# Kernel optimization log

Measured on AMD Instinct MI355X. Metric: run time of the kernel, lower is better.

## Reference

```python
import jax, jax.numpy as jnp
import numpy as np

B, L, C, R = 64, 2048, 512, 64
EPS_NORM = 1e-12
EPS_LN = 1e-5


def setup_inputs() -> dict:
    key = jax.random.key(0)
    ks = jax.random.split(key, 12)
    s_in = 1.0 / np.sqrt(L)
    s_r = 1.0 / np.sqrt(R)
    return {
        "x": jax.random.normal(ks[0], (B, L, C), dtype=jnp.float32),
        "Wd": jax.random.uniform(ks[1], (R, L), jnp.float32, -s_in, s_in),
        "bd": jax.random.uniform(ks[2], (R,), jnp.float32, -s_in, s_in),
        "Wq": jax.random.uniform(ks[3], (R, R), jnp.float32, -s_r, s_r),
        "Wk": jax.random.uniform(ks[4], (R, R), jnp.float32, -s_r, s_r),
        "Wv": jax.random.uniform(ks[5], (R, R), jnp.float32, -s_r, s_r),
        "Wg": jax.random.uniform(ks[6], (R, R), jnp.float32, -s_r, s_r),
        "bg": jax.random.uniform(ks[7], (R,), jnp.float32, -s_r, s_r),
        "Wu": jax.random.uniform(ks[8], (L, R), jnp.float32, -s_r, s_r),
        "bu": jax.random.uniform(ks[9], (L,), jnp.float32, -s_r, s_r),
        "gamma": jnp.ones((C,), jnp.float32),
        "beta": jnp.zeros((C,), jnp.float32),
        "alpha": jnp.asarray(0.1, jnp.float32),
    }


def _l2norm(t):
    # F.normalize(p=2, dim=-1): x / max(||x||, eps)
    n = jnp.sqrt(jnp.sum(t * t, axis=-1, keepdims=True))
    return t / jnp.maximum(n, EPS_NORM)


def reference(x, Wd, bd, Wq, Wk, Wv, Wg, bg, Wu, bu, gamma, beta, alpha):
    h = jnp.swapaxes(x, 1, 2)                      # (B, C, L): C tokens, L features
    h_low = jnp.einsum('bcl,rl->bcr', h, Wd) + bd  # (B, C, R)
    Q = _l2norm(jnp.einsum('bcr,sr->bcs', h_low, Wq))
    K = _l2norm(jnp.einsum('bcr,sr->bcs', h_low, Wk))
    V = jnp.einsum('bcr,sr->bcs', h_low, Wv)
    global_feat = jnp.sum(K * V, axis=1, keepdims=True)  # (B, 1, R)
    h_attn = Q * global_feat
    gate = jax.nn.sigmoid(jnp.einsum('bcr,sr->bcs', h_low, Wg) + bg)
    h_attn = h_attn * gate
    h_mixed = jnp.einsum('bcr,lr->bcl', h_attn, Wu) + bu  # (B, C, L)
    out = h + alpha * h_mixed
    out = jnp.swapaxes(out, 1, 2)                  # (B, L, C)
    mu = jnp.mean(out, axis=-1, keepdims=True)
    var = jnp.mean((out - mu) ** 2, axis=-1, keepdims=True)
    return (out - mu) / jnp.sqrt(var + EPS_LN) * gamma + beta
```

## Files before the change

### kernel.cpp

```cpp
#include <hip/hip_runtime.h>
#include <hip/hip_bf16.h>
#include <math.h>

#define B_ 64
#define L_ 2048
#define C_ 512
#define R_ 64
#define TL 16

#define BM 128
#define BK 32
#define LDK 36

typedef __attribute__((ext_vector_type(8))) short bf16x8;
typedef __attribute__((ext_vector_type(4))) float f32x4;

static __device__ __forceinline__ unsigned pkbf(float a, float b) {
    __hip_bfloat162 t = __float22bfloat162_rn(make_float2(a, b));
    union { __hip_bfloat162 h; unsigned u; } cv;
    cv.h = t;
    return cv.u;
}

__global__ void k_cast_wd(const float* __restrict__ Wd,
                          __hip_bfloat16* __restrict__ Wt) {
    int i = blockIdx.x * 256 + threadIdx.x;
    Wt[i] = __float2bfloat16(Wd[i]);
}

__global__ __launch_bounds__(256) void k_hlow_mfma(
        const float* __restrict__ x,
        const __hip_bfloat16* __restrict__ Wt,
        float* __restrict__ hlT) {
    __shared__ float xs[BM][LDK];

    const int tid  = threadIdx.x;
    const int lane = tid & 63;
    const int wv   = tid >> 6;
    const int quad = lane >> 4;
    const int mrow = lane & 15;

    const int c0     = blockIdx.x * BM;
    const int l_base = blockIdx.y * (L_ / 2);
    const int b      = blockIdx.z;

    const int cs = tid & 127;
    const int lh = (tid >> 7) * 16;

    f32x4 acc[2][4];
#pragma unroll
    for (int mt = 0; mt < 2; ++mt)
#pragma unroll
        for (int nt = 0; nt < 4; ++nt)
#pragma unroll
            for (int e = 0; e < 4; ++e) acc[mt][nt][e] = 0.f;

    const float* xptr = x + ((size_t)b * L_ + l_base + lh) * C_ + c0 + cs;
    const __hip_bfloat16* wbase = Wt + l_base + quad * 8;

    for (int kc = 0; kc < L_ / 2; kc += BK) {
        float v[16];
#pragma unroll
        for (int i = 0; i < 16; ++i) v[i] = xptr[(size_t)(kc + i) * C_];

        bf16x8 bfr[4];
#pragma unroll
        for (int nt = 0; nt < 4; ++nt)
            bfr[nt] = *reinterpret_cast<const bf16x8*>(
                wbase + (size_t)(nt * 16 + mrow) * L_ + kc);

        __syncthreads();
#pragma unroll
        for (int i = 0; i < 16; i += 4)
            *reinterpret_cast<float4*>(&xs[cs][lh + i]) =
                make_float4(v[i], v[i + 1], v[i + 2], v[i + 3]);
        __syncthreads();

#pragma unroll
        for (int mt = 0; mt < 2; ++mt) {
            const float* ap = &xs[wv * 32 + mt * 16 + mrow][quad * 8];
            float4 lo = *reinterpret_cast<const float4*>(ap);
            float4 hi = *reinterpret_cast<const float4*>(ap + 4);
            union { bf16x8 v8; unsigned u[4]; } af;
            af.u[0] = pkbf(lo.x, lo.y);
            af.u[1] = pkbf(lo.z, lo.w);
            af.u[2] = pkbf(hi.x, hi.y);
            af.u[3] = pkbf(hi.z, hi.w);
#pragma unroll
            for (int nt = 0; nt < 4; ++nt)
                acc[mt][nt] = __builtin_amdgcn_mfma_f32_16x16x32_bf16(
                    af.v8, bfr[nt], acc[mt][nt], 0, 0, 0);
        }
    }

#pragma unroll
    for (int mt = 0; mt < 2; ++mt)
#pragma unroll
        for (int nt = 0; nt < 4; ++nt) {
            const int rg = nt * 16 + mrow;
            const int cg = c0 + wv * 32 + mt * 16 + quad * 4;
#pragma unroll
            for (int e = 0; e < 4; ++e)
                atomicAdd(&hlT[((size_t)b * R_ + rg) * C_ + cg + e],
                          acc[mt][nt][e]);
        }
}

__global__ __launch_bounds__(256) void k_qkvg(
        const float* __restrict__ hlT,
        const float* __restrict__ bd,
        const float* __restrict__ Wq,
        const float* __restrict__ Wk,
        const float* __restrict__ Wv,
        const float* __restrict__ Wg,
        const float* __restrict__ bg,
        float* __restrict__ PT,
        float* __restrict__ G) {
    const int lane = threadIdx.x & 63;
    const int wv   = threadIdx.x >> 6;
    const int c    = blockIdx.x * 64 + lane;
    const int b    = blockIdx.y;

    float h[R_];
#pragma unroll
    for (int r = 0; r < R_; ++r)
        h[r] = hlT[((size_t)b * R_ + r) * C_ + c] + bd[r];

    float sq = 0.f, sk = 0.f;
#pragma unroll 4
    for (int i = 0; i < 16; ++i) {
        const int s = wv * 16 + i;
        const float4* wq4 = reinterpret_cast<const float4*>(Wq + s * R_);
        const float4* wk4 = reinterpret_cast<const float4*>(Wk + s * R_);
        float q = 0.f, k = 0.f;
#pragma unroll
        for (int j = 0; j < R_ / 4; ++j) {
            float4 a = wq4[j], d = wk4[j];
            float h0 = h[4 * j], h1 = h[4 * j + 1], h2 = h[4 * j + 2], h3 = h[4 * j + 3];
            q += h0 * a.x + h1 * a.y + h2 * a.z + h3 * a.w;
            k += h0 * d.x + h1 * d.y + h2 * d.z + h3 * d.w;
        }
        sq += q * q;
        sk += k * k;
    }

    __shared__ float rq[4][64], rk[4][64];
    rq[wv][lane] = sq;
    rk[wv][lane] = sk;
    __syncthreads();
    sq = rq[0][lane] + rq[1][lane] + rq[2][lane] + rq[3][lane];
    sk = rk[0][lane] + rk[1][lane] + rk[2][lane] + rk[3][lane];
    const float inq = 1.f / fmaxf(sqrtf(sq), 1e-12f);
    const float ink = 1.f / fmaxf(sqrtf(sk), 1e-12f);

#pragma unroll 2
    for (int i = 0; i < 16; ++i) {
        const int s = wv * 16 + i;
        const float4* wq4 = reinterpret_cast<const float4*>(Wq + s * R_);
        const float4* wk4 = reinterpret_cast<const float4*>(Wk + s * R_);
        const float4* wv4 = reinterpret_cast<const float4*>(Wv + s * R_);
        const float4* wg4 = reinterpret_cast<const float4*>(Wg + s * R_);
        float q = 0.f, k = 0.f, v = 0.f, g = 0.f;
#pragma unroll
        for (int j = 0; j < R_ / 4; ++j) {
            float4 a = wq4[j], d = wk4[j], e = wv4[j], f = wg4[j];
            float h0 = h[4 * j], h1 = h[4 * j + 1], h2 = h[4 * j + 2], h3 = h[4 * j + 3];
            q += h0 * a.x + h1 * a.y + h2 * a.z + h3 * a.w;
            k += h0 * d.x + h1 * d.y + h2 * d.z + h3 * d.w;
            v += h0 * e.x + h1 * e.y + h2 * e.z + h3 * e.w;
            g += h0 * f.x + h1 * f.y + h2 * f.z + h3 * f.w;
        }
        const float gate = 1.f / (1.f + expf(-(g + bg[s])));
        PT[((size_t)b * R_ + s) * C_ + c] = q * inq * gate;

        float kv = (k * ink) * v;
#pragma unroll
        for (int off = 32; off > 0; off >>= 1) kv += __shfl_xor(kv, off, 64);
        if (lane == 0) atomicAdd(&G[b * R_ + s], kv);
    }
}

__global__ __launch_bounds__(512) void k_out(const float* __restrict__ x,
                                             const float* __restrict__ PT,
                                             const float* __restrict__ G,
                                             const float* __restrict__ Wu,
                                             const float* __restrict__ bu,
                                             const float* __restrict__ gamma,
                                             const float* __restrict__ beta,
                                             const float* __restrict__ alpha_p,
                                             float* __restrict__ out) {
    const int c  = threadIdx.x;
    const int b  = blockIdx.y;
    const int l0 = blockIdx.x * TL;
    const float alpha = alpha_p[0];

    float ha[R_];
#pragma unroll
    for (int r = 0; r < R_; ++r)
        ha[r] = PT[((size_t)b * R_ + r) * C_ + c] * G[b * R_ + r];

    float vals[TL];
#pragma unroll
    for (int lt = 0; lt < TL; ++lt) {
        const int l = l0 + lt;
        const float4* wu4 = reinterpret_cast<const float4*>(Wu + l * R_);
        float m = 0.f;
#pragma unroll
        for (int i = 0; i < R_ / 4; ++i) {
            float4 w = wu4[i];
            m += ha[4 * i] * w.x + ha[4 * i + 1] * w.y + ha[4 * i + 2] * w.z + ha[4 * i + 3] * w.w;
        }
        vals[lt] = x[((size_t)b * L_ + l) * C_ + c] + alpha * (m + bu[l]);
    }

    __shared__ float2 redLds[TL][8];
    __shared__ float2 mvLds[TL];
    const int lane = c & 63, wv = c >> 6;
#pragma unroll
    for (int lt = 0; lt < TL; ++lt) {
        float s = vals[lt], s2 = vals[lt] * vals[lt];
#pragma unroll
        for (int off = 32; off > 0; off >>= 1) {
            s  += __shfl_xor(s, off, 64);
            s2 += __shfl_xor(s2, off, 64);
        }
        if (lane == 0) redLds[lt][wv] = make_float2(s, s2);
    }
    __syncthreads();
    if (threadIdx.x < TL) {
        float s = 0.f, s2 = 0.f;
#pragma unroll
        for (int w = 0; w < 8; ++w) {
            s  += redLds[threadIdx.x][w].x;
            s2 += redLds[threadIdx.x][w].y;
        }
        const float mean = s * (1.f / C_);
        const float var  = s2 * (1.f / C_) - mean * mean;
        mvLds[threadIdx.x] = make_float2(mean, rsqrtf(var + 1e-5f));
    }
    __syncthreads();
    const float gm = gamma[c], bt = beta[c];
#pragma unroll
    for (int lt = 0; lt < TL; ++lt) {
        float2 mv = mvLds[lt];
        out[((size_t)b * L_ + (l0 + lt)) * C_ + c] = (vals[lt] - mv.x) * mv.y * gm + bt;
    }
}

extern "C" void kernel_launch(void* const* d_in, const int* in_sizes, int n_in,
                              void* d_out, int out_size, void* d_ws, size_t ws_size,
                              hipStream_t stream) {
    const float* x     = (const float*)d_in[0];
    const float* Wd    = (const float*)d_in[1];
    const float* bd    = (const float*)d_in[2];
    const float* Wq    = (const float*)d_in[3];
    const float* Wk    = (const float*)d_in[4];
    const float* Wv    = (const float*)d_in[5];
    const float* Wg    = (const float*)d_in[6];
    const float* bg    = (const float*)d_in[7];
    const float* Wu    = (const float*)d_in[8];
    const float* bu    = (const float*)d_in[9];
    const float* gamma = (const float*)d_in[10];
    const float* beta  = (const float*)d_in[11];
    const float* alpha = (const float*)d_in[12];
    float* out = (float*)d_out;

    char* ws = (char*)d_ws;
    __hip_bfloat16* Wt = (__hip_bfloat16*)ws;
    float* hlT = (float*)(ws + (512 << 10));
    float* PT  = (float*)(ws + (512 << 10) + (8 << 20));
    float* G   = (float*)(ws + (512 << 10) + (16 << 20));

    k_cast_wd<<<dim3((R_ * L_) / 256), 256, 0, stream>>>(Wd, Wt);
    hipMemsetAsync(hlT, 0, (size_t)B_ * R_ * C_ * sizeof(float), stream);
    hipMemsetAsync(G, 0, B_ * R_ * sizeof(float), stream);
    k_hlow_mfma<<<dim3(C_ / BM, 2, B_), 256, 0, stream>>>(x, Wt, hlT);
    k_qkvg<<<dim3(C_ / 64, B_), 256, 0, stream>>>(hlT, bd, Wq, Wk, Wv, Wg, bg, PT, G);
    k_out<<<dim3(L_ / TL, B_), 512, 0, stream>>>(x, PT, G, Wu, bu, gamma, beta, alpha, out);
}
```

Before: 804.7 us.

## Use bf16 MFMA for up-projection, transpose intermediates, split L across more blocks

The output kernel now computes the up-projection with bf16 MFMA instructions, using a pre-cast bf16 copy of Wu, instead of a scalar fp32 dot-product loop per thread. The h_low and P intermediates are stored row-major (C by R) so loads can be vectorised. The down-projection split-K grows from 2 to 8 slices to expose more parallelism, at the cost of more atomic adds. The qkvg kernel is restructured so each thread computes 8 output features with a single pass over the weights. The bf16 rounding of P·G and Wu adds some numerical error.

Result: faster. 741.2 us (-7.9%).

```diff
diff --git a/kernel.cpp b/kernel.cpp
--- a/kernel.cpp
+++ b/kernel.cpp
@@ -11,6 +11,8 @@
 #define BM 128
 #define BK 32
 #define LDK 36
+#define NSL 8
+#define LSL (L_ / NSL)
 
 typedef __attribute__((ext_vector_type(8))) short bf16x8;
 typedef __attribute__((ext_vector_type(4))) float f32x4;
@@ -22,16 +24,19 @@
     return cv.u;
 }
 
-__global__ void k_cast_wd(const float* __restrict__ Wd,
-                          __hip_bfloat16* __restrict__ Wt) {
+__global__ void k_cast(const float* __restrict__ Wd,
+                       const float* __restrict__ Wu,
+                       __hip_bfloat16* __restrict__ Wt,
+                       __hip_bfloat16* __restrict__ Wub) {
     int i = blockIdx.x * 256 + threadIdx.x;
-    Wt[i] = __float2bfloat16(Wd[i]);
+    if (i < R_ * L_) Wt[i] = __float2bfloat16(Wd[i]);
+    else             Wub[i - R_ * L_] = __float2bfloat16(Wu[i - R_ * L_]);
 }
 
 __global__ __launch_bounds__(256) void k_hlow_mfma(
         const float* __restrict__ x,
         const __hip_bfloat16* __restrict__ Wt,
-        float* __restrict__ hlT) {
+        float* __restrict__ hl) {
     __shared__ float xs[BM][LDK];
 
     const int tid  = threadIdx.x;
@@ -41,7 +46,7 @@
     const int mrow = lane & 15;
 
     const int c0     = blockIdx.x * BM;
-    const int l_base = blockIdx.y * (L_ / 2);
+    const int l_base = blockIdx.y * LSL;
     const int b      = blockIdx.z;
 
     const int cs = tid & 127;
@@ -58,7 +63,7 @@
     const float* xptr = x + ((size_t)b * L_ + l_base + lh) * C_ + c0 + cs;
     const __hip_bfloat16* wbase = Wt + l_base + quad * 8;
 
-    for (int kc = 0; kc < L_ / 2; kc += BK) {
+    for (int kc = 0; kc < LSL; kc += BK) {
         float v[16];
 #pragma unroll
         for (int i = 0; i < 16; ++i) v[i] = xptr[(size_t)(kc + i) * C_];
@@ -101,149 +106,198 @@
             const int cg = c0 + wv * 32 + mt * 16 + quad * 4;
 #pragma unroll
             for (int e = 0; e < 4; ++e)
-                atomicAdd(&hlT[((size_t)b * R_ + rg) * C_ + cg + e],
+                atomicAdd(&hl[((size_t)b * C_ + cg + e) * R_ + rg],
                           acc[mt][nt][e]);
         }
 }
 
 __global__ __launch_bounds__(256) void k_qkvg(
-        const float* __restrict__ hlT,
+        const float* __restrict__ hl,
         const float* __restrict__ bd,
         const float* __restrict__ Wq,
         const float* __restrict__ Wk,
         const float* __restrict__ Wv,
         const float* __restrict__ Wg,
         const float* __restrict__ bg,
-        float* __restrict__ PT,
+        float* __restrict__ P,
         float* __restrict__ G) {
-    const int lane = threadIdx.x & 63;
-    const int wv   = threadIdx.x >> 6;
-    const int c    = blockIdx.x * 64 + lane;
-    const int b    = blockIdx.y;
-
-    float h[R_];
-#pragma unroll
-    for (int r = 0; r < R_; ++r)
-        h[r] = hlT[((size_t)b * R_ + r) * C_ + c] + bd[r];
+    const int tid = threadIdx.x;
+    const int ci  = tid & 31;
+    const int sg  = tid >> 5;
+    const int wv  = tid >> 6;
+    const int c   = blockIdx.x * 32 + ci;
+    const int b   = blockIdx.y;
+    const int s0  = sg * 8;
+    const float* hrow = hl + ((size_t)b * C_ + c) * R_;
+
+    float q[8], k[8], v[8], g[8];
+#pragma unroll
+    for (int i = 0; i < 8; ++i) { q[i] = 0.f; k[i] = 0.f; v[i] = 0.f; g[i] = 0.f; }
+
+#pragma unroll 1
+    for (int jc = 0; jc < 4; ++jc) {
+        float hc[16];
+        const float4* h4 = reinterpret_cast<const float4*>(hrow + jc * 16);
+        const float4* b4 = reinterpret_cast<const float4*>(bd + jc * 16);
+#pragma unroll
+        for (int t = 0; t < 4; ++t) {
+            float4 hv = h4[t], bv = b4[t];
+            hc[4 * t + 0] = hv.x + bv.x;
+            hc[4 * t + 1] = hv.y + bv.y;
+            hc[4 * t + 2] = hv.z + bv.z;
+            hc[4 * t + 3] = hv.w + bv.w;
+        }
+#pragma unroll
+        for (int i = 0; i < 8; ++i) {
+            const float4* wq4 = reinterpret_cast<const float4*>(Wq + (size_t)(s0 + i) * R_ + jc * 16);
+            const float4* wk4 = reinterpret_cast<const float4*>(Wk + (size_t)(s0 + i) * R_ + jc * 16);
+            const float4* wv4 = reinterpret_cast<const float4*>(Wv + (size_t)(s0 + i) * R_ + jc * 16);
+            const float4* wg4 = reinterpret_cast<const float4*>(Wg + (size_t)(s0 + i) * R_ + jc * 16);
+#pragma unroll
+            for (int t = 0; t < 4; ++t) {
+                float4 a = wq4[t], d = wk4[t], e2 = wv4[t], f = wg4[t];
+                float h0 = hc[4 * t], h1 = hc[4 * t + 1], h2 = hc[4 * t + 2], h3 = hc[4 * t + 3];
+                q[i] += h0 * a.x  + h1 * a.y  + h2 * a.z  + h3 * a.w;
+                k[i] += h0 * d.x  + h1 * d.y  + h2 * d.z  + h3 * d.w;
+                v[i] += h0 * e2.x + h1 * e2.y + h2 * e2.z + h3 * e2.w;
+                g[i] += h0 * f.x  + h1 * f.y  + h2 * f.z  + h3 * f.w;
+            }
+        }
+    }
 
     float sq = 0.f, sk = 0.f;
-#pragma unroll 4
-    for (int i = 0; i < 16; ++i) {
-        const int s = wv * 16 + i;
-        const float4* wq4 = reinterpret_cast<const float4*>(Wq + s * R_);
-        const float4* wk4 = reinterpret_cast<const float4*>(Wk + s * R_);
-        float q = 0.f, k = 0.f;
-#pragma unroll
-        for (int j = 0; j < R_ / 4; ++j) {
-            float4 a = wq4[j], d = wk4[j];
-            float h0 = h[4 * j], h1 = h[4 * j + 1], h2 = h[4 * j + 2], h3 = h[4 * j + 3];
-            q += h0 * a.x + h1 * a.y + h2 * a.z + h3 * a.w;
-            k += h0 * d.x + h1 * d.y + h2 * d.z + h3 * d.w;
-        }
-        sq += q * q;
-        sk += k * k;
-    }
-
-    __shared__ float rq[4][64], rk[4][64];
-    rq[wv][lane] = sq;
-    rk[wv][lane] = sk;
+#pragma unroll
+    for (int i = 0; i < 8; ++i) { sq += q[i] * q[i]; sk += k[i] * k[i]; }
+    sq += __shfl_xor(sq, 32, 64);
+    sk += __shfl_xor(sk, 32, 64);
+    __shared__ float rqs[4][32], rks[4][32];
+    if ((tid & 32) == 0) { rqs[wv][ci] = sq; rks[wv][ci] = sk; }
     __syncthreads();
-    sq = rq[0][lane] + rq[1][lane] + rq[2][lane] + rq[3][lane];
-    sk = rk[0][lane] + rk[1][lane] + rk[2][lane] + rk[3][lane];
+    sq = rqs[0][ci] + rqs[1][ci] + rqs[2][ci] + rqs[3][ci];
+    sk = rks[0][ci] + rks[1][ci] + rks[2][ci] + rks[3][ci];
     const float inq = 1.f / fmaxf(sqrtf(sq), 1e-12f);
     const float ink = 1.f / fmaxf(sqrtf(sk), 1e-12f);
 
-#pragma unroll 2
-    for (int i = 0; i < 16; ++i) {
-        const int s = wv * 16 + i;
-        const float4* wq4 = reinterpret_cast<const float4*>(Wq + s * R_);
-        const float4* wk4 = reinterpret_cast<const float4*>(Wk + s * R_);
-        const float4* wv4 = reinterpret_cast<const float4*>(Wv + s * R_);
-        const float4* wg4 = reinterpret_cast<const float4*>(Wg + s * R_);
-        float q = 0.f, k = 0.f, v = 0.f, g = 0.f;
-#pragma unroll
-        for (int j = 0; j < R_ / 4; ++j) {
-            float4 a = wq4[j], d = wk4[j], e = wv4[j], f = wg4[j];
-            float h0 = h[4 * j], h1 = h[4 * j + 1], h2 = h[4 * j + 2], h3 = h[4 * j + 3];
-            q += h0 * a.x + h1 * a.y + h2 * a.z + h3 * a.w;
-            k += h0 * d.x + h1 * d.y + h2 * d.z + h3 * d.w;
-            v += h0 * e.x + h1 * e.y + h2 * e.z + h3 * e.w;
-            g += h0 * f.x + h1 * f.y + h2 * f.z + h3 * f.w;
-        }
-        const float gate = 1.f / (1.f + expf(-(g + bg[s])));
-        PT[((size_t)b * R_ + s) * C_ + c] = q * inq * gate;
-
-        float kv = (k * ink) * v;
-#pragma unroll
-        for (int off = 32; off > 0; off >>= 1) kv += __shfl_xor(kv, off, 64);
-        if (lane == 0) atomicAdd(&G[b * R_ + s], kv);
-    }
+    float pv[8], kv[8];
+#pragma unroll
+    for (int i = 0; i < 8; ++i) {
+        const float gate = 1.f / (1.f + expf(-(g[i] + bg[s0 + i])));
+        pv[i] = q[i] * inq * gate;
+        kv[i] = (k[i] * ink) * v[i];
+    }
+    float* prow = P + ((size_t)b * C_ + c) * R_ + s0;
+    *reinterpret_cast<float4*>(prow)     = make_float4(pv[0], pv[1], pv[2], pv[3]);
+    *reinterpret_cast<float4*>(prow + 4) = make_float4(pv[4], pv[5], pv[6], pv[7]);
+
+#pragma unroll
+    for (int off = 1; off < 32; off <<= 1)
+#pragma unroll
+        for (int i = 0; i < 8; ++i) kv[i] += __shfl_xor(kv[i], off, 64);
+    if (ci == 0)
+#pragma unroll
+        for (int i = 0; i < 8; ++i) atomicAdd(&G[b * R_ + s0 + i], kv[i]);
 }
 
 __global__ __launch_bounds__(512) void k_out(const float* __restrict__ x,
-                                             const float* __restrict__ PT,
+                                             const float* __restrict__ P,
                                              const float* __restrict__ G,
-                                             const float* __restrict__ Wu,
+                                             const __hip_bfloat16* __restrict__ Wub,
                                              const float* __restrict__ bu,
                                              const float* __restrict__ gamma,
                                              const float* __restrict__ beta,
                                              const float* __restrict__ alpha_p,
                                              float* __restrict__ out) {
-    const int c  = threadIdx.x;
-    const int b  = blockIdx.y;
-    const int l0 = blockIdx.x * TL;
+    const int tid  = threadIdx.x;
+    const int lane = tid & 63;
+    const int wv   = tid >> 6;
+    const int n16  = lane & 15;
+    const int quad = lane >> 4;
+    const int b    = blockIdx.y;
+    const int l0   = blockIdx.x * TL;
     const float alpha = alpha_p[0];
 
-    float ha[R_];
-#pragma unroll
-    for (int r = 0; r < R_; ++r)
-        ha[r] = PT[((size_t)b * R_ + r) * C_ + c] * G[b * R_ + r];
-
-    float vals[TL];
-#pragma unroll
-    for (int lt = 0; lt < TL; ++lt) {
-        const int l = l0 + lt;
-        const float4* wu4 = reinterpret_cast<const float4*>(Wu + l * R_);
-        float m = 0.f;
-#pragma unroll
-        for (int i = 0; i < R_ / 4; ++i) {
-            float4 w = wu4[i];
-            m += ha[4 * i] * w.x + ha[4 * i + 1] * w.y + ha[4 * i + 2] * w.z + ha[4 * i + 3] * w.w;
-        }
-        vals[lt] = x[((size_t)b * L_ + l) * C_ + c] + alpha * (m + bu[l]);
-    }
-
-    __shared__ float2 redLds[TL][8];
-    __shared__ float2 mvLds[TL];
-    const int lane = c & 63, wv = c >> 6;
-#pragma unroll
-    for (int lt = 0; lt < TL; ++lt) {
-        float s = vals[lt], s2 = vals[lt] * vals[lt];
-#pragma unroll
-        for (int off = 32; off > 0; off >>= 1) {
+    const __hip_bfloat16* wrow = Wub + (size_t)(l0 + n16) * R_ + quad * 8;
+    const bf16x8 af0 = *reinterpret_cast<const bf16x8*>(wrow);
+    const bf16x8 af1 = *reinterpret_cast<const bf16x8*>(wrow + 32);
+
+    const float* gp = G + b * R_ + quad * 8;
+    const float4 ga0 = *reinterpret_cast<const float4*>(gp);
+    const float4 ga1 = *reinterpret_cast<const float4*>(gp + 4);
+    const float4 gb0 = *reinterpret_cast<const float4*>(gp + 32);
+    const float4 gb1 = *reinterpret_cast<const float4*>(gp + 36);
+
+    f32x4 acc[4];
+#pragma unroll
+    for (int nt = 0; nt < 4; ++nt)
+#pragma unroll
+        for (int e = 0; e < 4; ++e) acc[nt][e] = 0.f;
+
+    const int cb = wv * 64;
+#pragma unroll
+    for (int nt = 0; nt < 4; ++nt) {
+        const float* prow = P + ((size_t)b * C_ + cb + nt * 16 + n16) * R_ + quad * 8;
+        float4 p0 = *reinterpret_cast<const float4*>(prow);
+        float4 p1 = *reinterpret_cast<const float4*>(prow + 4);
+        union { bf16x8 v8; unsigned u[4]; } bf;
+        bf.u[0] = pkbf(p0.x * ga0.x, p0.y * ga0.y);
+        bf.u[1] = pkbf(p0.z * ga0.z, p0.w * ga0.w);
+        bf.u[2] = pkbf(p1.x * ga1.x, p1.y * ga1.y);
+        bf.u[3] = pkbf(p1.z * ga1.z, p1.w * ga1.w);
+        acc[nt] = __builtin_amdgcn_mfma_f32_16x16x32_bf16(af0, bf.v8, acc[nt], 0, 0, 0);
+        float4 q0 = *reinterpret_cast<const float4*>(prow + 32);
+        float4 q1 = *reinterpret_cast<const float4*>(prow + 36);
+        bf.u[0] = pkbf(q0.x * gb0.x, q0.y * gb0.y);
+        bf.u[1] = pkbf(q0.z * gb0.z, q0.w * gb0.w);
+        bf.u[2] = pkbf(q1.x * gb1.x, q1.y * gb1.y);
+        bf.u[3] = pkbf(q1.z * gb1.z, q1.w * gb1.w);
+        acc[nt] = __builtin_amdgcn_mfma_f32_16x16x32_bf16(af1, bf.v8, acc[nt], 0, 0, 0);
+    }
+
+    float ab[4];
+#pragma unroll
+    for (int e = 0; e < 4; ++e) ab[e] = alpha * bu[l0 + quad * 4 + e];
+    const float* xrow = x + ((size_t)b * L_ + l0 + quad * 4) * C_ + cb + n16;
+    float vals[4][4];
+#pragma unroll
+    for (int nt = 0; nt < 4; ++nt)
+#pragma unroll
+        for (int e = 0; e < 4; ++e)
+            vals[nt][e] = xrow[(size_t)e * C_ + nt * 16] + alpha * acc[nt][e] + ab[e];
+
+    __shared__ float2 red[TL][8];
+    __shared__ float2 mv[TL];
+#pragma unroll
+    for (int e = 0; e < 4; ++e) {
+        float s  = vals[0][e] + vals[1][e] + vals[2][e] + vals[3][e];
+        float s2 = vals[0][e] * vals[0][e] + vals[1][e] * vals[1][e]
+                 + vals[2][e] * vals[2][e] + vals[3][e] * vals[3][e];
+#pragma unroll
+        for (int off = 1; off < 16; off <<= 1) {
             s  += __shfl_xor(s, off, 64);
             s2 += __shfl_xor(s2, off, 64);
         }
-        if (lane == 0) redLds[lt][wv] = make_float2(s, s2);
+        if (n16 == 0) red[quad * 4 + e][wv] = make_float2(s, s2);
     }
     __syncthreads();
-    if (threadIdx.x < TL) {
+    if (tid < TL) {
         float s = 0.f, s2 = 0.f;
 #pragma unroll
-        for (int w = 0; w < 8; ++w) {
-            s  += redLds[threadIdx.x][w].x;
-            s2 += redLds[threadIdx.x][w].y;
-        }
+        for (int w = 0; w < 8; ++w) { s += red[tid][w].x; s2 += red[tid][w].y; }
         const float mean = s * (1.f / C_);
         const float var  = s2 * (1.f / C_) - mean * mean;
-        mvLds[threadIdx.x] = make_float2(mean, rsqrtf(var + 1e-5f));
+        mv[tid] = make_float2(mean, rsqrtf(var + 1e-5f));
     }
     __syncthreads();
-    const float gm = gamma[c], bt = beta[c];
-#pragma unroll
-    for (int lt = 0; lt < TL; ++lt) {
-        float2 mv = mvLds[lt];
-        out[((size_t)b * L_ + (l0 + lt)) * C_ + c] = (vals[lt] - mv.x) * mv.y * gm + bt;
+    float* orow = out + ((size_t)b * L_ + l0 + quad * 4) * C_ + cb + n16;
+#pragma unroll
+    for (int nt = 0; nt < 4; ++nt) {
+        const int c = cb + nt * 16 + n16;
+        const float gm = gamma[c], bt = beta[c];
+#pragma unroll
+        for (int e = 0; e < 4; ++e) {
+            const float2 m = mv[quad * 4 + e];
+            orow[(size_t)e * C_ + nt * 16] = (vals[nt][e] - m.x) * m.y * gm + bt;
+        }
     }
 }
 
@@ -266,15 +320,16 @@
     float* out = (float*)d_out;
 
     char* ws = (char*)d_ws;
-    __hip_bfloat16* Wt = (__hip_bfloat16*)ws;
-    float* hlT = (float*)(ws + (512 << 10));
-    float* PT  = (float*)(ws + (512 << 10) + (8 << 20));
-    float* G   = (float*)(ws + (512 << 10) + (16 << 20));
-
-    k_cast_wd<<<dim3((R_ * L_) / 256), 256, 0, stream>>>(Wd, Wt);
-    hipMemsetAsync(hlT, 0, (size_t)B_ * R_ * C_ * sizeof(float), stream);
+    __hip_bfloat16* Wt  = (__hip_bfloat16*)ws;
+    __hip_bfloat16* Wub = (__hip_bfloat16*)(ws + (256 << 10));
+    float* hl = (float*)(ws + (512 << 10));
+    float* P  = (float*)(ws + (512 << 10) + (8 << 20));
+    float* G  = (float*)(ws + (512 << 10) + (16 << 20));
+
+    k_cast<<<dim3((2 * R_ * L_) / 256), 256, 0, stream>>>(Wd, Wu, Wt, Wub);
+    hipMemsetAsync(hl, 0, (size_t)B_ * C_ * R_ * sizeof(float), stream);
     hipMemsetAsync(G, 0, B_ * R_ * sizeof(float), stream);
-    k_hlow_mfma<<<dim3(C_ / BM, 2, B_), 256, 0, stream>>>(x, Wt, hlT);
-    k_qkvg<<<dim3(C_ / 64, B_), 256, 0, stream>>>(hlT, bd, Wq, Wk, Wv, Wg, bg, PT, G);
-    k_out<<<dim3(L_ / TL, B_), 512, 0, stream>>>(x, PT, G, Wu, bu, gamma, beta, alpha, out);
-}
+    k_hlow_mfma<<<dim3(C_ / BM, NSL, B_), 256, 0, stream>>>(x, Wt, hl);
+    k_qkvg<<<dim3(C_ / 32, B_), 256, 0, stream>>>(hl, bd, Wq, Wk, Wv, Wg, bg, P, G);
+    k_out<<<dim3(L_ / TL, B_), 512, 0, stream>>>(x, P, G, Wub, bu, gamma, beta, alpha, out);
+}
```
